# Kernel optimization log

Measured on AMD Instinct MI355X. Metric: run time of the kernel, lower is better.

The kernel has to match this reference:

```python
import jax, jax.numpy as jnp
import numpy as np

B, H, W, C = 8, 112, 112, 192
NH = 6
HD = C // NH
WS = 7            # window size
SS = 3            # shift size (WS//2)
N = WS * WS       # tokens per window (49)
NW = (H // WS) * (W // WS)  # windows per image
EPS = 1e-5
LOG100 = float(np.log(100.0))


def _rel_bias_consts():
    # continuous relative coords table, shape ((2*WS-1)^2, 2), log-spaced
    r = np.arange(-(WS - 1), WS, dtype=np.float32)
    table = np.stack(np.meshgrid(r, r, indexing='ij')).transpose(1, 2, 0).reshape(-1, 2)
    table = table / float(max(WS - 1, 1)) * 8.0
    table = np.sign(table) * np.log2(np.abs(table) + 1.0) / np.log2(8.0)
    # relative position index, shape (N*N,)
    coords = np.stack(np.meshgrid(np.arange(WS), np.arange(WS), indexing='ij')).reshape(2, -1)
    rel = (coords[:, :, None] - coords[:, None, :]).transpose(1, 2, 0) + (WS - 1)
    idx = (rel * np.array([2 * WS - 1, 1])).sum(-1).astype(np.int32).reshape(-1)
    return jnp.asarray(table), jnp.asarray(idx)


def _shift_attn_mask():
    # standard Swin shifted-window attention mask, shape (NW, N, N)
    img = np.zeros((H, W), np.float32)
    cnt = 0
    for hs in (slice(0, -WS), slice(-WS, -SS), slice(-SS, None)):
        for ws_ in (slice(0, -WS), slice(-WS, -SS), slice(-SS, None)):
            img[hs, ws_] = cnt
            cnt += 1
    win = img.reshape(H // WS, WS, W // WS, WS).transpose(0, 2, 1, 3).reshape(-1, N)
    diff = win[:, None, :] - win[:, :, None]
    return jnp.asarray(np.where(diff != 0, -100.0, 0.0).astype(np.float32))


_TABLE, _IDX = _rel_bias_consts()
_MASK = _shift_attn_mask()


def _ln(x, g, b):
    m = jnp.mean(x, axis=-1, keepdims=True)
    v = jnp.mean((x - m) ** 2, axis=-1, keepdims=True)
    return (x - m) / jnp.sqrt(v + EPS) * g + b


def setup_inputs() -> dict:
    key = jax.random.key(0)
    ks = jax.random.split(key, 8)
    s = 0.02
    return {
        'x': jax.random.normal(ks[0], (B, H * W, C), jnp.float32),
        'ln1_g': jnp.ones((C,), jnp.float32), 'ln1_b': jnp.zeros((C,), jnp.float32),
        'ln2_g': jnp.ones((C,), jnp.float32), 'ln2_b': jnp.zeros((C,), jnp.float32),
        'q_w': jax.random.normal(ks[1], (C, C), jnp.float32) * s,
        'q_b': jnp.zeros((C,), jnp.float32),
        'k_w': jax.random.normal(ks[2], (C, C), jnp.float32) * s,
        'v_w': jax.random.normal(ks[3], (C, C), jnp.float32) * s,
        'v_b': jnp.zeros((C,), jnp.float32),
        'p_w': jax.random.normal(ks[4], (C, C), jnp.float32) * s,
        'p_b': jnp.zeros((C,), jnp.float32),
        'logit_scale': jnp.log(10.0 * jnp.ones((NH, 1, 1), jnp.float32)),
        'cpb_w0': jax.random.normal(ks[5], (2, 512), jnp.float32) * s,
        'cpb_b0': jnp.zeros((512,), jnp.float32),
        'cpb_w1': jax.random.normal(ks[6], (512, NH), jnp.float32) * s,
        'fc1_w': jax.random.normal(ks[7], (C, 4 * C), jnp.float32) * s,
        'fc1_b': jnp.zeros((4 * C,), jnp.float32),
        'fc2_w': jax.random.normal(jax.random.fold_in(key, 9), (4 * C, C), jnp.float32) * s,
        'fc2_b': jnp.zeros((C,), jnp.float32),
    }


def reference(x, ln1_g, ln1_b, ln2_g, ln2_b, q_w, q_b, k_w, v_w, v_b, p_w, p_b,
              logit_scale, cpb_w0, cpb_b0, cpb_w1, fc1_w, fc1_b, fc2_w, fc2_b):
    shortcut = x
    h = x.reshape(B, H, W, C)
    h = jnp.roll(h, (-SS, -SS), axis=(1, 2))                       # cyclic shift
    # window partition -> (B*NW, N, C)
    win = h.reshape(B, H // WS, WS, W // WS, WS, C).transpose(0, 1, 3, 2, 4, 5)
    win = win.reshape(B * NW, N, C)

    q = (win @ q_w + q_b).reshape(-1, N, NH, HD).transpose(0, 2, 1, 3)  # (BW,h,N,d)
    k = (win @ k_w).reshape(-1, N, NH, HD).transpose(0, 2, 1, 3)
    v = (win @ v_w + v_b).reshape(-1, N, NH, HD).transpose(0, 2, 1, 3)

    # cosine attention with learned clamped logit scale
    qn = q / jnp.maximum(jnp.linalg.norm(q, axis=-1, keepdims=True), 1e-12)
    kn = k / jnp.maximum(jnp.linalg.norm(k, axis=-1, keepdims=True), 1e-12)
    scale = jnp.exp(jnp.minimum(logit_scale, LOG100))              # (h,1,1)
    attn = jnp.einsum('whqd,whkd->whqk', qn, kn) * scale

    # continuous relative position bias: MLP(2->512->h), gather, 16*sigmoid
    t = jax.nn.relu(_TABLE @ cpb_w0 + cpb_b0) @ cpb_w1             # ((2WS-1)^2, h)
    bias = t[_IDX].reshape(N, N, NH).transpose(2, 0, 1)            # (h,N,N)
    attn = attn + 16.0 * jax.nn.sigmoid(bias)[None]

    # shifted-window mask
    attn = attn.reshape(B, NW, NH, N, N) + _MASK[None, :, None]
    attn = jax.nn.softmax(attn.reshape(B * NW, NH, N, N), axis=-1)

    out = jnp.einsum('whqk,whkd->whqd', attn, v)                   # (BW,h,N,d)
    out = out.transpose(0, 2, 1, 3).reshape(B * NW, N, C)
    out = out @ p_w + p_b

    # window reverse + un-shift
    out = out.reshape(B, H // WS, W // WS, WS, WS, C).transpose(0, 1, 3, 2, 4, 5)
    out = out.reshape(B, H, W, C)
    out = jnp.roll(out, (SS, SS), axis=(1, 2)).reshape(B, H * W, C)

    # swin-v2 res-post-norm residuals
    hidden = shortcut + _ln(out, ln1_g, ln1_b)
    mlp = jax.nn.gelu(hidden @ fc1_w + fc1_b) @ fc2_w + fc2_b
    return hidden + _ln(mlp, ln2_g, ln2_b)
```

## Files before the change

kernel.cpp:

```cpp
#include <hip/hip_runtime.h>


typedef __bf16  bf16x8 __attribute__((ext_vector_type(8)));
typedef float   f32x4  __attribute__((ext_vector_type(4)));

__device__ __forceinline__ float bf2f(unsigned short u){
    return __uint_as_float(((unsigned int)u) << 16);
}
__device__ __forceinline__ unsigned short f2bf(float f){
    unsigned int u = __float_as_uint(f);
    unsigned int r = (u + 0x7fffu + ((u >> 16) & 1u)) >> 16;
    return (unsigned short)r;
}
__device__ __forceinline__ float ldin(const void* p, size_t i, int f32){
    return f32 ? ((const float*)p)[i] : bf2f(((const unsigned short*)p)[i]);
}

__global__ void detect_kernel(const unsigned short* __restrict__ ln1g, int* __restrict__ flag){
    if (threadIdx.x == 0) *flag = (ln1g[0] == 0x3F80u) ? 0 : 1;
}

__global__ __launch_bounds__(256)
void pack_kernel(const void* __restrict__ qw, const void* __restrict__ kw,
                 const void* __restrict__ vw, const void* __restrict__ qb,
                 const void* __restrict__ vb, const void* __restrict__ pw,
                 const void* __restrict__ pb, const void* __restrict__ f1w,
                 const void* __restrict__ f1b, const void* __restrict__ f2w,
                 const void* __restrict__ f2b,
                 const void* __restrict__ l1g, const void* __restrict__ l1b,
                 const void* __restrict__ l2g, const void* __restrict__ l2b,
                 unsigned short* __restrict__ wqkvt, unsigned short* __restrict__ pwt,
                 unsigned short* __restrict__ f1t, unsigned short* __restrict__ f2t,
                 float* __restrict__ qkv_bias, float* __restrict__ p_bias,
                 float* __restrict__ f1_bias, float* __restrict__ f2_bias,
                 float* __restrict__ lnp, const int* __restrict__ dtf)
{
    int f32 = *dtf;
    int i = blockIdx.x * 256 + threadIdx.x;
    if (i < 110592){
        int n = i / 192, k = i - n * 192;
        float s = (n < 192) ? ldin(qw, (size_t)k*192 + n, f32)
                 : (n < 384) ? ldin(kw, (size_t)k*192 + (n-192), f32)
                 : ldin(vw, (size_t)k*192 + (n-384), f32);
        wqkvt[n*192 + k] = f2bf(s);
    }
    if (i < 36864){
        int n = i / 192, k = i - n * 192;
        pwt[n*192 + k] = f2bf(ldin(pw, (size_t)k*192 + n, f32));
    }
    if (i < 147456){
        int n = i / 192, k = i - n * 192;
        f1t[n*192 + k] = f2bf(ldin(f1w, (size_t)k*768 + n, f32));
        int n2 = i / 768, k2 = i - n2 * 768;
        f2t[n2*768 + k2] = f2bf(ldin(f2w, (size_t)k2*192 + n2, f32));
    }
    if (i < 576) qkv_bias[i] = (i < 192) ? ldin(qb, i, f32)
                              : (i < 384) ? 0.f : ldin(vb, i-384, f32);
    if (i < 192){
        p_bias[i]  = ldin(pb, i, f32);
        f2_bias[i] = ldin(f2b, i, f32);
        lnp[i]       = ldin(l1g, i, f32);
        lnp[192+i]   = ldin(l1b, i, f32);
        lnp[384+i]   = ldin(l2g, i, f32);
        lnp[576+i]   = ldin(l2b, i, f32);
    }
    if (i < 768) f1_bias[i] = ldin(f1b, i, f32);
}

__device__ __forceinline__ float cpb_coord(int a){
    float v = (float)(a - 6) * (8.0f / 6.0f);
    float s = (v > 0.f) ? 1.f : (v < 0.f ? -1.f : 0.f);
    return s * log2f(fabsf(v) + 1.f) * (1.f / 3.f);
}

__global__ __launch_bounds__(256)
void cpb_kernel(const void* __restrict__ ls, const void* __restrict__ w0,
                const void* __restrict__ b0, const void* __restrict__ w1,
                float* __restrict__ bmask, float* __restrict__ scale,
                const int* __restrict__ dtf)
{
    __shared__ float w0a[512], w0b[512], b0s[512], w1s[512];
    __shared__ float tv[169];
    __shared__ float sval[2401];
    int f32 = *dtf;
    int tid = threadIdx.x;
    int h = blockIdx.x;

    for (int c = tid; c < 512; c += 256){
        w0a[c] = ldin(w0, c, f32);
        w0b[c] = ldin(w0, 512 + c, f32);
        b0s[c] = ldin(b0, c, f32);
        w1s[c] = ldin(w1, (size_t)c*6 + h, f32);
    }
    __syncthreads();

    for (int q = tid; q < 169; q += 256){
        int a = q / 13, b = q - a * 13;
        float t0 = cpb_coord(a), t1 = cpb_coord(b);
        float acc = 0.f;
        for (int c = 0; c < 512; ++c){
            float hv = fmaxf(t0 * w0a[c] + t1 * w0b[c] + b0s[c], 0.f);
            acc += hv * w1s[c];
        }
        tv[q] = acc;
    }
    __syncthreads();

    for (int e = tid; e < 2401; e += 256){
        int i = e / 49, j = e - i * 49;
        int di = i/7 - j/7 + 6;
        int dj = (i - (i/7)*7) - (j - (j/7)*7) + 6;
        sval[e] = 16.f / (1.f + expf(-tv[di*13 + dj]));
    }
    __syncthreads();

    for (int t = 0; t < 4; ++t){
        int ey = t >> 1, ex = t & 1;
        for (int e = tid; e < 4096; e += 256){
            int row = e >> 6, li = e & 63;
            int lrow = li >> 2, f = li & 3;
            int col = f*16 + lrow;
            float val;
            if (row >= 49) val = 0.f;
            else if (col >= 49) val = -1e30f;
            else {
                val = sval[row*49 + col];
                int rr = row/7, rc = row - rr*7;
                int cr = col/7, cc = col - cr*7;
                int ridr = (ey ? (rr < 4 ? 1 : 2) : 0)*3 + (ex ? (rc < 4 ? 1 : 2) : 0);
                int ridc = (ey ? (cr < 4 ? 1 : 2) : 0)*3 + (ex ? (cc < 4 ? 1 : 2) : 0);
                if (ridr != ridc) val -= 100.f;
            }
            bmask[(((size_t)(h*4 + t)*64 + row) << 6) + li] = val;
        }
    }
    if (tid == 0) scale[h] = expf(fminf(ldin(ls, h, f32), 4.6051702f));
}

template<int GATHER, int EPI>
__global__ __launch_bounds__(256)
void gemm_kernel(const void* __restrict__ A,
                 const unsigned short* __restrict__ Bt,
                 const float* __restrict__ bias,
                 unsigned short* __restrict__ Cout,
                 int M, int N, int K, const int* __restrict__ dtf)
{
    __shared__ unsigned short As[64][40];
    __shared__ unsigned short Bs[3][64][40];

    int f32 = GATHER ? *dtf : 0;
    int tid = threadIdx.x;
    int nb = N / 192;
    int bng = blockIdx.x % nb;
    int bm  = (blockIdx.x / nb) * 64;
    int bn0 = bng * 192;
    int arow = tid >> 2, aseg = tid & 3;

    size_t aoff;
    if (GATHER){
        int t = bm + arow;
        int w = t / 49, p = t - w * 49;
        int bb = w >> 8, widx = w & 255;
        int wy = widx >> 4, wx = widx & 15;
        int r = p / 7, c = p - r * 7;
        int oy = (wy*7 + r + 3) % 112;
        int ox = (wx*7 + c + 3) % 112;
        aoff = ((size_t)bb * 12544 + (size_t)oy * 112 + ox) * 192;
    } else {
        aoff = (size_t)(bm + arow) * K;
    }
    const unsigned short* brp0 = Bt + (size_t)(bn0       + arow) * K;
    const unsigned short* brp1 = Bt + (size_t)(bn0 +  64 + arow) * K;
    const unsigned short* brp2 = Bt + (size_t)(bn0 + 128 + arow) * K;

    int wave = tid >> 6, lane = tid & 63;
    int wm = (wave >> 1) * 32, wn = (wave & 1) * 32;
    int quad = lane >> 4, lrow = lane & 15;

    f32x4 acc[3][2][2] = {};

    for (int k0 = 0; k0 < K; k0 += 32){
        __syncthreads();
        if (GATHER && f32){
            const float* p = (const float*)A + aoff + k0 + aseg*8;
            unsigned short t8[8];
            #pragma unroll
            for (int j = 0; j < 8; ++j) t8[j] = f2bf(p[j]);
            *(uint4*)(&As[arow][aseg*8]) = *(const uint4*)t8;
        } else {
            *(uint4*)(&As[arow][aseg*8]) =
                *(const uint4*)((const unsigned short*)A + aoff + k0 + aseg*8);
        }
        *(uint4*)(&Bs[0][arow][aseg*8]) = *(const uint4*)(brp0 + k0 + aseg*8);
        *(uint4*)(&Bs[1][arow][aseg*8]) = *(const uint4*)(brp1 + k0 + aseg*8);
        *(uint4*)(&Bs[2][arow][aseg*8]) = *(const uint4*)(brp2 + k0 + aseg*8);
        __syncthreads();
        bf16x8 a0 = *(const bf16x8*)(&As[wm      + lrow][quad*8]);
        bf16x8 a1 = *(const bf16x8*)(&As[wm + 16 + lrow][quad*8]);
        #pragma unroll
        for (int nt = 0; nt < 3; ++nt){
            bf16x8 b0 = *(const bf16x8*)(&Bs[nt][wn      + lrow][quad*8]);
            bf16x8 b1 = *(const bf16x8*)(&Bs[nt][wn + 16 + lrow][quad*8]);
            acc[nt][0][0] = __builtin_amdgcn_mfma_f32_16x16x32_bf16(a0, b0, acc[nt][0][0], 0, 0, 0);
            acc[nt][0][1] = __builtin_amdgcn_mfma_f32_16x16x32_bf16(a0, b1, acc[nt][0][1], 0, 0, 0);
            acc[nt][1][0] = __builtin_amdgcn_mfma_f32_16x16x32_bf16(a1, b0, acc[nt][1][0], 0, 0, 0);
            acc[nt][1][1] = __builtin_amdgcn_mfma_f32_16x16x32_bf16(a1, b1, acc[nt][1][1], 0, 0, 0);
        }
    }

    #pragma unroll
    for (int nt = 0; nt < 3; ++nt)
    for (int tm = 0; tm < 2; ++tm)
    for (int tn = 0; tn < 2; ++tn)
    #pragma unroll
    for (int i = 0; i < 4; ++i){
        int row = bm + wm + tm*16 + quad*4 + i;
        int col = bn0 + nt*64 + wn + tn*16 + lrow;
        float v = acc[nt][tm][tn][i] + bias[col];
        if (EPI == 1){
            float t = __expf(v * fmaf(v*v, -0.071354816f, -1.5957691216f));
            v = v * __builtin_amdgcn_rcpf(1.f + t);
        }
        Cout[(size_t)row * N + col] = f2bf(v);
    }
}

__global__ __launch_bounds__(256)
void attn_kernel(const unsigned short* __restrict__ qkv,
                 const float* __restrict__ bmask,
                 const float* __restrict__ scale,
                 unsigned short* __restrict__ attn_out)
{
    __shared__ unsigned short qb[64][40];
    __shared__ unsigned short kb[64][40];
    __shared__ unsigned short vT[32][72];
    __shared__ unsigned short Ps[64][72];
    __shared__ float rnq[64], rnk[64];

    int tid = threadIdx.x;
    int w = blockIdx.x, h = blockIdx.y;
    int widx = w & 255;
    int wy = widx >> 4, wx = widx & 15;
    int mtype = ((wy == 15) ? 2 : 0) | ((wx == 15) ? 1 : 0);

    size_t wbase = (size_t)w * 49 * 576 + (size_t)h * 32;

    for (int e = tid; e < 392; e += 256){
        int p = e >> 3, s = e & 7;
        size_t g = wbase + (size_t)p * 576 + s * 4;
        *(uint2*)&qb[p][s*4] = *(const uint2*)&qkv[g];
        *(uint2*)&kb[p][s*4] = *(const uint2*)&qkv[g + 192];
    }
    for (int e = tid; e < 480; e += 256){
        int p = 49 + (e >> 5), d = e & 31;
        qb[p][d] = 0; kb[p][d] = 0;
    }
    for (int e = tid; e < 1568; e += 256){
        int p = e >> 5, d = e & 31;
        vT[d][p] = qkv[wbase + (size_t)p * 576 + 384 + d];
    }
    for (int e = tid; e < 480; e += 256){
        int d = e / 15, j = 49 + (e - d * 15);
        vT[d][j] = 0;
    }
    __syncthreads();

    for (int e = tid; e < 1568; e += 256){
        int p = e >> 5, d = e & 31;
        float qv = bf2f(qb[p][d]), kv = bf2f(kb[p][d]);
        float q2 = qv*qv, k2 = kv*kv;
        #pragma unroll
        for (int m = 16; m; m >>= 1){ q2 += __shfl_xor(q2, m); k2 += __shfl_xor(k2, m); }
        if (d == 0){
            rnq[p] = 1.f / fmaxf(sqrtf(q2), 1e-12f);
            rnk[p] = 1.f / fmaxf(sqrtf(k2), 1e-12f);
        }
    }
    __syncthreads();

    int wave = tid >> 6, lane = tid & 63;
    int quad = lane >> 4, lrow = lane & 15;
    int wm = wave * 16;

    bf16x8 aq = *(const bf16x8*)&qb[wm + lrow][quad * 8];
    f32x4 sfr[4];
    #pragma unroll
    for (int f = 0; f < 4; ++f){
        bf16x8 bk = *(const bf16x8*)&kb[f*16 + lrow][quad * 8];
        f32x4 z = {0.f, 0.f, 0.f, 0.f};
        sfr[f] = __builtin_amdgcn_mfma_f32_16x16x32_bf16(aq, bk, z, 0, 0, 0);
    }

    float sc = scale[h];
    float rk[4];
    #pragma unroll
    for (int f = 0; f < 4; ++f) rk[f] = rnk[f*16 + lrow];
    const float4* bmp = (const float4*)bmask + (size_t)(h*4 + mtype) * 1024;
    #pragma unroll
    for (int reg = 0; reg < 4; ++reg){
        int row = wm + quad*4 + reg;
        float rq = rnq[row] * sc;
        float4 bm = bmp[row*16 + lrow];
        float v0 = fmaf(sfr[0][reg], rq*rk[0], bm.x);
        float v1 = fmaf(sfr[1][reg], rq*rk[1], bm.y);
        float v2 = fmaf(sfr[2][reg], rq*rk[2], bm.z);
        float v3 = fmaf(sfr[3][reg], rq*rk[3], bm.w);
        float mx = fmaxf(fmaxf(v0, v1), fmaxf(v2, v3));
        #pragma unroll
        for (int m = 8; m; m >>= 1) mx = fmaxf(mx, __shfl_xor(mx, m));
        float e0 = __expf(v0 - mx), e1 = __expf(v1 - mx);
        float e2 = __expf(v2 - mx), e3 = __expf(v3 - mx);
        float sm = (e0 + e1) + (e2 + e3);
        #pragma unroll
        for (int m = 8; m; m >>= 1) sm += __shfl_xor(sm, m);
        float inv = 1.f / sm;
        Ps[row][ 0 + lrow] = f2bf(e0 * inv);
        Ps[row][16 + lrow] = f2bf(e1 * inv);
        Ps[row][32 + lrow] = f2bf(e2 * inv);
        Ps[row][48 + lrow] = f2bf(e3 * inv);
    }
    __syncthreads();

    f32x4 o[2] = {{0.f,0.f,0.f,0.f}, {0.f,0.f,0.f,0.f}};
    #pragma unroll
    for (int c = 0; c < 2; ++c){
        bf16x8 ap = *(const bf16x8*)&Ps[wm + lrow][c*32 + quad*8];
        #pragma unroll
        for (int n = 0; n < 2; ++n){
            bf16x8 bv = *(const bf16x8*)&vT[n*16 + lrow][c*32 + quad*8];
            o[n] = __builtin_amdgcn_mfma_f32_16x16x32_bf16(ap, bv, o[n], 0, 0, 0);
        }
    }
    __syncthreads();

    unsigned short (*Os)[40] = qb;
    #pragma unroll
    for (int n = 0; n < 2; ++n)
    #pragma unroll
    for (int reg = 0; reg < 4; ++reg){
        int row = wm + quad*4 + reg;
        if (row < 49) Os[row][n*16 + lrow] = f2bf(o[n][reg]);
    }
    __syncthreads();

    for (int e = tid; e < 392; e += 256){
        int p = e >> 3, c4 = (e & 7) * 4;
        uint2 val = *(const uint2*)&Os[p][c4];
        *(uint2*)&attn_out[((size_t)w*49 + p)*192 + (size_t)h*32 + c4] = val;
    }
}

template<int FINAL>
__global__ __launch_bounds__(256)
void ln_kernel(const void* __restrict__ base,
               const unsigned short* __restrict__ src,
               const float* __restrict__ g,
               const float* __restrict__ b,
               void* __restrict__ dst, const int* __restrict__ dtf)
{
    int f32 = *dtf;
    int tid = threadIdx.x;
    int lane = tid & 63;
    int token = blockIdx.x * 4 + (tid >> 6);

    size_t srow;
    if (FINAL){
        srow = (size_t)token * 192;
    } else {
        int bb = token / 12544, pix = token - bb*12544;
        int y = pix / 112, x = pix - y*112;
        int gy = (y + 109) % 112, gx = (x + 109) % 112;
        int wy = gy / 7, r = gy - wy*7;
        int wx = gx / 7, c = gx - wx*7;
        int t = (bb*256 + wy*16 + wx)*49 + r*7 + c;
        srow = (size_t)t * 192;
    }

    float o[3]; float s = 0.f;
    #pragma unroll
    for (int j = 0; j < 3; ++j){ o[j] = bf2f(src[srow + j*64 + lane]); s += o[j]; }
    #pragma unroll
    for (int off = 32; off; off >>= 1) s += __shfl_xor(s, off);
    float m = s * (1.f/192.f);
    float vsum = 0.f;
    #pragma unroll
    for (int j = 0; j < 3; ++j){ float d = o[j] - m; vsum += d*d; }
    #pragma unroll
    for (int off = 32; off; off >>= 1) vsum += __shfl_xor(vsum, off);
    float rstd = rsqrtf(vsum * (1.f/192.f) + 1e-5f);

    size_t brow = (size_t)token * 192;
    #pragma unroll
    for (int j = 0; j < 3; ++j){
        int cidx = j*64 + lane;
        float bv = FINAL ? bf2f(((const unsigned short*)base)[brow + cidx])
                         : ldin(base, brow + cidx, f32);
        float val = bv + (o[j] - m) * rstd * g[cidx] + b[cidx];
        if (FINAL){
            if (f32) ((float*)dst)[brow + cidx] = val;
            else     ((unsigned short*)dst)[brow + cidx] = f2bf(val);
        } else {
            ((unsigned short*)dst)[brow + cidx] = f2bf(val);
        }
    }
}

extern "C" void kernel_launch(void* const* d_in, const int* in_sizes, int n_in,
                              void* d_out, int out_size, void* d_ws, size_t ws_size,
                              hipStream_t stream)
{
    const void* x    = d_in[0];
    const void* ln1g = d_in[1];
    const void* ln1b = d_in[2];
    const void* ln2g = d_in[3];
    const void* ln2b = d_in[4];
    const void* qw   = d_in[5];
    const void* qb   = d_in[6];
    const void* kw   = d_in[7];
    const void* vw   = d_in[8];
    const void* vb   = d_in[9];
    const void* pw   = d_in[10];
    const void* pb   = d_in[11];
    const void* ls   = d_in[12];
    const void* w0   = d_in[13];
    const void* b0   = d_in[14];
    const void* w1   = d_in[15];
    const void* f1w  = d_in[16];
    const void* f1b  = d_in[17];
    const void* f2w  = d_in[18];
    const void* f2b  = d_in[19];

    char* ws = (char*)d_ws;
    unsigned short* big    = (unsigned short*)(ws);
    unsigned short* bufB   = (unsigned short*)(ws + 154140672);
    unsigned short* hidden = (unsigned short*)(ws + 192675840);
    unsigned short* wqkvt  = (unsigned short*)(ws + 231211008);
    unsigned short* pwt    = (unsigned short*)(ws + 231211008 + 221184);
    unsigned short* f1t    = (unsigned short*)(ws + 231211008 + 221184 + 73728);
    unsigned short* f2t    = (unsigned short*)(ws + 231211008 + 221184 + 73728 + 294912);
    float* qkv_bias = (float*)(ws + 232095744);
    float* p_bias   = qkv_bias + 576;
    float* f1_bias  = p_bias + 192;
    float* f2_bias  = f1_bias + 768;
    float* bmask    = (float*)(ws + 232102656);
    float* scale    = (float*)(ws + 232495872);
    float* lnp      = (float*)(ws + 232495896);
    int*   dtf      = (int*)  (ws + 232498968);

    detect_kernel<<<1, 64, 0, stream>>>((const unsigned short*)ln1g, dtf);
    pack_kernel<<<576, 256, 0, stream>>>(qw, kw, vw, qb, vb, pw, pb, f1w, f1b, f2w, f2b,
                                         ln1g, ln1b, ln2g, ln2b,
                                         wqkvt, pwt, f1t, f2t,
                                         qkv_bias, p_bias, f1_bias, f2_bias, lnp, dtf);
    cpb_kernel<<<6, 256, 0, stream>>>(ls, w0, b0, w1, bmask, scale, dtf);

    gemm_kernel<1,0><<<1568*3, 256, 0, stream>>>(x, wqkvt, qkv_bias, big, 100352, 576, 192, dtf);
    attn_kernel<<<dim3(2048, 6), 256, 0, stream>>>(big, bmask, scale, bufB);
    gemm_kernel<0,0><<<1568, 256, 0, stream>>>(bufB, pwt, p_bias, big, 100352, 192, 192, dtf);
    ln_kernel<0><<<25088, 256, 0, stream>>>(x, big, lnp, lnp + 192, hidden, dtf);
    gemm_kernel<0,1><<<1568*4, 256, 0, stream>>>(hidden, f1t, f1_bias, big, 100352, 768, 192, dtf);
    gemm_kernel<0,0><<<1568, 256, 0, stream>>>(big, f2t, f2_bias, bufB, 100352, 192, 768, dtf);
    ln_kernel<1><<<25088, 256, 0, stream>>>(hidden, bufB, lnp + 384, lnp + 576, d_out, dtf);

    (void)in_sizes; (void)n_in; (void)out_size; (void)ws_size;
}
```

Measured before the change: 593.2 us.

## Enlarge GEMM block tile to 128x192 with per-wave full-width N strips

Doubles the GEMM block tile in M from 64 to 128 rows while keeping 192 columns. Each of the four waves now owns a 32x192 strip and reuses its two A fragments across twelve B fragments. This halves the grid size and raises arithmetic intensity per LDS load, cutting repeated B-tile loads from global memory. In exchange each thread holds twice as many accumulator registers (96 floats), which may lower occupancy, and the grid is coarser.

```diff
diff --git a/kernel.cpp b/kernel.cpp
--- a/kernel.cpp
+++ b/kernel.cpp
@@ -145,78 +145,86 @@
                  unsigned short* __restrict__ Cout,
                  int M, int N, int K, const int* __restrict__ dtf)
 {
-    __shared__ unsigned short As[64][40];
-    __shared__ unsigned short Bs[3][64][40];
+    __shared__ unsigned short As[128][40];
+    __shared__ unsigned short Bs[192][40];
 
     int f32 = GATHER ? *dtf : 0;
     int tid = threadIdx.x;
     int nb = N / 192;
     int bng = blockIdx.x % nb;
-    int bm  = (blockIdx.x / nb) * 64;
+    int bm  = (blockIdx.x / nb) * 128;
     int bn0 = bng * 192;
     int arow = tid >> 2, aseg = tid & 3;
 
-    size_t aoff;
+    size_t aoff0, aoff1;
     if (GATHER){
-        int t = bm + arow;
-        int w = t / 49, p = t - w * 49;
-        int bb = w >> 8, widx = w & 255;
-        int wy = widx >> 4, wx = widx & 15;
-        int r = p / 7, c = p - r * 7;
-        int oy = (wy*7 + r + 3) % 112;
-        int ox = (wx*7 + c + 3) % 112;
-        aoff = ((size_t)bb * 12544 + (size_t)oy * 112 + ox) * 192;
+        #pragma unroll
+        for (int half = 0; half < 2; ++half){
+            int t = bm + arow + half*64;
+            int w = t / 49, p = t - w * 49;
+            int bb = w >> 8, widx = w & 255;
+            int wy = widx >> 4, wx = widx & 15;
+            int r = p / 7, c = p - r * 7;
+            int oy = (wy*7 + r + 3) % 112;
+            int ox = (wx*7 + c + 3) % 112;
+            size_t ao = ((size_t)bb * 12544 + (size_t)oy * 112 + ox) * 192;
+            if (half == 0) aoff0 = ao; else aoff1 = ao;
+        }
     } else {
-        aoff = (size_t)(bm + arow) * K;
+        aoff0 = (size_t)(bm + arow) * K;
+        aoff1 = (size_t)(bm + arow + 64) * K;
     }
     const unsigned short* brp0 = Bt + (size_t)(bn0       + arow) * K;
     const unsigned short* brp1 = Bt + (size_t)(bn0 +  64 + arow) * K;
     const unsigned short* brp2 = Bt + (size_t)(bn0 + 128 + arow) * K;
 
     int wave = tid >> 6, lane = tid & 63;
-    int wm = (wave >> 1) * 32, wn = (wave & 1) * 32;
+    int wm = wave * 32;
     int quad = lane >> 4, lrow = lane & 15;
 
-    f32x4 acc[3][2][2] = {};
+    f32x4 acc[12][2] = {};
 
     for (int k0 = 0; k0 < K; k0 += 32){
         __syncthreads();
         if (GATHER && f32){
-            const float* p = (const float*)A + aoff + k0 + aseg*8;
+            const float* p0 = (const float*)A + aoff0 + k0 + aseg*8;
+            const float* p1 = (const float*)A + aoff1 + k0 + aseg*8;
             unsigned short t8[8];
             #pragma unroll
-            for (int j = 0; j < 8; ++j) t8[j] = f2bf(p[j]);
+            for (int j = 0; j < 8; ++j) t8[j] = f2bf(p0[j]);
             *(uint4*)(&As[arow][aseg*8]) = *(const uint4*)t8;
+            #pragma unroll
+            for (int j = 0; j < 8; ++j) t8[j] = f2bf(p1[j]);
+            *(uint4*)(&As[arow + 64][aseg*8]) = *(const uint4*)t8;
         } else {
             *(uint4*)(&As[arow][aseg*8]) =
-                *(const uint4*)((const unsigned short*)A + aoff + k0 + aseg*8);
-        }
-        *(uint4*)(&Bs[0][arow][aseg*8]) = *(const uint4*)(brp0 + k0 + aseg*8);
-        *(uint4*)(&Bs[1][arow][aseg*8]) = *(const uint4*)(brp1 + k0 + aseg*8);
-        *(uint4*)(&Bs[2][arow][aseg*8]) = *(const uint4*)(brp2 + k0 + aseg*8);
+                *(const uint4*)((const unsigned short*)A + aoff0 + k0 + aseg*8);
+            *(uint4*)(&As[arow + 64][aseg*8]) =
+                *(const uint4*)((const unsigned short*)A + aoff1 + k0 + aseg*8);
+        }
+        *(uint4*)(&Bs[arow      ][aseg*8]) = *(const uint4*)(brp0 + k0 + aseg*8);
+        *(uint4*)(&Bs[arow +  64][aseg*8]) = *(const uint4*)(brp1 + k0 + aseg*8);
+        *(uint4*)(&Bs[arow + 128][aseg*8]) = *(const uint4*)(brp2 + k0 + aseg*8);
         __syncthreads();
         bf16x8 a0 = *(const bf16x8*)(&As[wm      + lrow][quad*8]);
         bf16x8 a1 = *(const bf16x8*)(&As[wm + 16 + lrow][quad*8]);
         #pragma unroll
-        for (int nt = 0; nt < 3; ++nt){
-            bf16x8 b0 = *(const bf16x8*)(&Bs[nt][wn      + lrow][quad*8]);
-            bf16x8 b1 = *(const bf16x8*)(&Bs[nt][wn + 16 + lrow][quad*8]);
-            acc[nt][0][0] = __builtin_amdgcn_mfma_f32_16x16x32_bf16(a0, b0, acc[nt][0][0], 0, 0, 0);
-            acc[nt][0][1] = __builtin_amdgcn_mfma_f32_16x16x32_bf16(a0, b1, acc[nt][0][1], 0, 0, 0);
-            acc[nt][1][0] = __builtin_amdgcn_mfma_f32_16x16x32_bf16(a1, b0, acc[nt][1][0], 0, 0, 0);
-            acc[nt][1][1] = __builtin_amdgcn_mfma_f32_16x16x32_bf16(a1, b1, acc[nt][1][1], 0, 0, 0);
-        }
-    }
-
-    #pragma unroll
-    for (int nt = 0; nt < 3; ++nt)
+        for (int f = 0; f < 12; ++f){
+            bf16x8 bb = *(const bf16x8*)(&Bs[f*16 + lrow][quad*8]);
+            acc[f][0] = __builtin_amdgcn_mfma_f32_16x16x32_bf16(a0, bb, acc[f][0], 0, 0, 0);
+            acc[f][1] = __builtin_amdgcn_mfma_f32_16x16x32_bf16(a1, bb, acc[f][1], 0, 0, 0);
+        }
+    }
+
+    #pragma unroll
+    for (int f = 0; f < 12; ++f)
+    #pragma unroll
     for (int tm = 0; tm < 2; ++tm)
-    for (int tn = 0; tn < 2; ++tn)
     #pragma unroll
     for (int i = 0; i < 4; ++i){
         int row = bm + wm + tm*16 + quad*4 + i;
-        int col = bn0 + nt*64 + wn + tn*16 + lrow;
-        float v = acc[nt][tm][tn][i] + bias[col];
+        int col = bn0 + f*16 + lrow;
+        float v = acc[f][tm][i] + bias[col];
         if (EPI == 1){
             float t = __expf(v * fmaf(v*v, -0.071354816f, -1.5957691216f));
             v = v * __builtin_amdgcn_rcpf(1.f + t);
@@ -454,12 +462,12 @@
                                          qkv_bias, p_bias, f1_bias, f2_bias, lnp, dtf);
     cpb_kernel<<<6, 256, 0, stream>>>(ls, w0, b0, w1, bmask, scale, dtf);
 
-    gemm_kernel<1,0><<<1568*3, 256, 0, stream>>>(x, wqkvt, qkv_bias, big, 100352, 576, 192, dtf);
+    gemm_kernel<1,0><<<784*3, 256, 0, stream>>>(x, wqkvt, qkv_bias, big, 100352, 576, 192, dtf);
     attn_kernel<<<dim3(2048, 6), 256, 0, stream>>>(big, bmask, scale, bufB);
-    gemm_kernel<0,0><<<1568, 256, 0, stream>>>(bufB, pwt, p_bias, big, 100352, 192, 192, dtf);
+    gemm_kernel<0,0><<<784, 256, 0, stream>>>(bufB, pwt, p_bias, big, 100352, 192, 192, dtf);
     ln_kernel<0><<<25088, 256, 0, stream>>>(x, big, lnp, lnp + 192, hidden, dtf);
-    gemm_kernel<0,1><<<1568*4, 256, 0, stream>>>(hidden, f1t, f1_bias, big, 100352, 768, 192, dtf);
-    gemm_kernel<0,0><<<1568, 256, 0, stream>>>(big, f2t, f2_bias, bufB, 100352, 192, 768, dtf);
+    gemm_kernel<0,1><<<784*4, 256, 0, stream>>>(hidden, f1t, f1_bias, big, 100352, 768, 192, dtf);
+    gemm_kernel<0,0><<<784, 256, 0, stream>>>(big, f2t, f2_bias, bufB, 100352, 192, 768, dtf);
     ln_kernel<1><<<25088, 256, 0, stream>>>(hidden, bufB, lnp + 384, lnp + 576, d_out, dtf);
 
     (void)in_sizes; (void)n_in; (void)out_size; (void)ws_size;
```

Result: no change. 587.8 us (-0.9%).
